# Performance work log

Hardware: AMD Instinct MI355X
Metric: run time of the kernel (lower is better)

The kernel has to match this reference:

```python
import jax, jax.numpy as jnp
import numpy as np

TAU_MEM = 20.0          # tau for both ExpLeak (syn) and LIF (mem)
SPIKE_THRESHOLD = 1.0
WIDTH_GRAD = 0.5        # surrogate gradient width (unused in fwd)
SCALE_GRAD = 1.0


def setup_inputs() -> dict:
    key = jax.random.key(0)
    k1, k2 = jax.random.split(key)
    x = jax.random.normal(k1, (32, 2048, 512, 1), dtype=jnp.float32)
    weight = jax.random.uniform(k2, (1, 1), dtype=jnp.float32)  # Linear(1,1,bias=False) weight (set to scalar `weight` in torch)
    return {"x": x, "weight": weight}


def reference(x, weight):
    # x: (B, T, N, 1); weight: (1, 1)
    alpha = jnp.exp(jnp.asarray(-1.0 / TAU_MEM, dtype=x.dtype))
    i_in = x * weight[0, 0]                      # Linear(1,1,no bias)
    i_in = jnp.moveaxis(i_in, 1, 0)              # (T, B, N, 1) for scan over time

    def step(carry, i_t):
        v_syn, v_mem = carry
        # ExpLeak, norm_input=False: v_syn = alpha*v_syn + input
        v_syn = alpha * v_syn + i_t
        # LIF, norm_input=False: decay then integrate synaptic current
        v_mem = alpha * v_mem + v_syn
        # SingleSpike: at most one spike per step
        spk = (v_mem >= SPIKE_THRESHOLD).astype(v_mem.dtype)
        # MembraneSubtract reset
        v_mem = v_mem - SPIKE_THRESHOLD * spk
        return (v_syn, v_mem), spk

    zeros = jnp.zeros_like(i_in[0])
    _, spikes = jax.lax.scan(step, (zeros, zeros), i_in)
    return jnp.moveaxis(spikes, 0, 1)            # (B, T, N, 1)
```

## Files before the change

kernel.cpp:

```cpp
#include <hip/hip_runtime.h>
#include <math.h>


constexpr int T_ = 2048;
constexpr int N_ = 512;
constexpr int TILE = 64;
constexpr int NTILE = T_ / TILE;
constexpr int NCH = 64;
constexpr int NBUF = 4;

typedef const __attribute__((address_space(1))) void* gas_ptr;
typedef __attribute__((address_space(3))) void* las_ptr;

__global__ __launch_bounds__(128, 1)
void exodus_dma2_kernel(const float* __restrict__ x,
                        const float* __restrict__ wptr,
                        float* __restrict__ out) {
    __shared__ float XBUF[NBUF][TILE][NCH];

    const int blk  = blockIdx.x;
    const int b    = blk >> 3;
    const int n0   = (blk & 7) * NCH;
    const int wave = threadIdx.x >> 6;
    const int lane = threadIdx.x & 63;

    if (wave == 1) {
        const int plane = lane >> 4;
        const int sub   = lane & 15;
        const float* __restrict__ gl =
            x + (size_t)b * T_ * N_ + (size_t)plane * N_ + n0 + sub * 4;

#define ISSUE_TILE(TT)                                                        \
        {                                                                     \
            const float* __restrict__ g_ =                                    \
                gl + (size_t)(TT) * TILE * N_;                                \
            _Pragma("unroll")                                                 \
            for (int j0_ = 0; j0_ < TILE; j0_ += 4) {                         \
                __builtin_amdgcn_global_load_lds(                             \
                    (gas_ptr)(g_ + (size_t)j0_ * N_),                         \
                    (las_ptr)&XBUF[(TT) & (NBUF - 1)][j0_][0], 16, 0, 0);     \
            }                                                                 \
        }

        ISSUE_TILE(0);
        ISSUE_TILE(1);
        __builtin_amdgcn_sched_barrier(0);
        asm volatile("s_waitcnt vmcnt(16)");
        __builtin_amdgcn_sched_barrier(0);
        __builtin_amdgcn_s_barrier();

        for (int t = 0; t < NTILE; ++t) {
            if (t + 2 < NTILE) {
                ISSUE_TILE(t + 2);
                __builtin_amdgcn_sched_barrier(0);
                asm volatile("s_waitcnt vmcnt(16)");
            } else {
                asm volatile("s_waitcnt vmcnt(0)");
            }
            __builtin_amdgcn_sched_barrier(0);
            __builtin_amdgcn_s_barrier();
        }
#undef ISSUE_TILE
    } else {
        const size_t base = (size_t)b * T_ * N_ + (size_t)n0 + lane;
        float* __restrict__ op = out + base;
        const float w = wptr[0];
        const float alpha = (float)exp((double)(-1.0f / 20.0f));
        float vsyn = 0.0f, vmem = 0.0f;

        __builtin_amdgcn_s_barrier();

        for (int t = 0; t < NTILE; ++t) {
            const int bb = t & (NBUF - 1);
            __builtin_amdgcn_sched_barrier(0);

            float xv[TILE];
#pragma unroll
            for (int j = 0; j < TILE; ++j) xv[j] = XBUF[bb][j][lane];

            float* __restrict__ o = op + (size_t)t * TILE * N_;
#pragma unroll
            for (int j = 0; j < TILE; ++j) {
                const float i_t = __fmul_rn(xv[j], w);
                vsyn = __fadd_rn(__fmul_rn(alpha, vsyn), i_t);
                const float va = __fadd_rn(__fmul_rn(alpha, vmem), vsyn);
                const bool fire = (va >= 1.0f);
                __builtin_nontemporal_store(fire ? 1.0f : 0.0f,
                                            o + (size_t)j * N_);
                vmem = fire ? __fsub_rn(va, 1.0f) : va;
            }
            __builtin_amdgcn_sched_barrier(0);
            __builtin_amdgcn_s_barrier();
        }
    }
}

extern "C" void kernel_launch(void* const* d_in, const int* in_sizes, int n_in,
                              void* d_out, int out_size, void* d_ws, size_t ws_size,
                              hipStream_t stream) {
    const float* x = (const float*)d_in[0];
    const float* w = (const float*)d_in[1];
    float* out = (float*)d_out;

    dim3 grid(256);
    dim3 block(128);
    hipLaunchKernelGGL(exodus_dma2_kernel, grid, block, 0, stream, x, w, out);
}
```

Before: 238.2 us.

## Add a dedicated store wave that writes spikes from LDS with float4 stores

Adds a third wave per block. The compute wave now writes spike values into a double-buffered LDS staging area instead of issuing per-element nontemporal global stores. The new wave reads the previous tile from LDS and writes it out as coalesced float4 stores, so stores overlap with compute of the next tile. This costs more LDS, a third wave, and an extra LDS round-trip, and the stores lose the nontemporal hint.

```diff
diff --git a/kernel.cpp b/kernel.cpp
--- a/kernel.cpp
+++ b/kernel.cpp
@@ -12,11 +12,12 @@
 typedef const __attribute__((address_space(1))) void* gas_ptr;
 typedef __attribute__((address_space(3))) void* las_ptr;
 
-__global__ __launch_bounds__(128, 1)
-void exodus_dma2_kernel(const float* __restrict__ x,
-                        const float* __restrict__ wptr,
-                        float* __restrict__ out) {
+__global__ __launch_bounds__(192, 1)
+void exodus_tri_kernel(const float* __restrict__ x,
+                       const float* __restrict__ wptr,
+                       float* __restrict__ out) {
     __shared__ float XBUF[NBUF][TILE][NCH];
+    __shared__ float SBUF[2][TILE][NCH];
 
     const int blk  = blockIdx.x;
     const int b    = blk >> 3;
@@ -61,9 +62,7 @@
             __builtin_amdgcn_s_barrier();
         }
 #undef ISSUE_TILE
-    } else {
-        const size_t base = (size_t)b * T_ * N_ + (size_t)n0 + lane;
-        float* __restrict__ op = out + base;
+    } else if (wave == 0) {
         const float w = wptr[0];
         const float alpha = (float)exp((double)(-1.0f / 20.0f));
         float vsyn = 0.0f, vmem = 0.0f;
@@ -71,26 +70,63 @@
         __builtin_amdgcn_s_barrier();
 
         for (int t = 0; t < NTILE; ++t) {
-            const int bb = t & (NBUF - 1);
+            const int xb = t & (NBUF - 1);
+            const int sb = t & 1;
             __builtin_amdgcn_sched_barrier(0);
 
             float xv[TILE];
 #pragma unroll
-            for (int j = 0; j < TILE; ++j) xv[j] = XBUF[bb][j][lane];
+            for (int j = 0; j < TILE; ++j) xv[j] = XBUF[xb][j][lane];
 
-            float* __restrict__ o = op + (size_t)t * TILE * N_;
 #pragma unroll
             for (int j = 0; j < TILE; ++j) {
                 const float i_t = __fmul_rn(xv[j], w);
                 vsyn = __fadd_rn(__fmul_rn(alpha, vsyn), i_t);
                 const float va = __fadd_rn(__fmul_rn(alpha, vmem), vsyn);
                 const bool fire = (va >= 1.0f);
-                __builtin_nontemporal_store(fire ? 1.0f : 0.0f,
-                                            o + (size_t)j * N_);
+                SBUF[sb][j][lane] = fire ? 1.0f : 0.0f;
                 vmem = fire ? __fsub_rn(va, 1.0f) : va;
             }
             __builtin_amdgcn_sched_barrier(0);
+            asm volatile("s_waitcnt lgkmcnt(0)");
+            __builtin_amdgcn_sched_barrier(0);
             __builtin_amdgcn_s_barrier();
+        }
+    } else {
+        const int plane = lane >> 4;
+        const int sub   = lane & 15;
+        float* __restrict__ ow =
+            out + (size_t)b * T_ * N_ + (size_t)plane * N_ + n0 + sub * 4;
+
+        __builtin_amdgcn_s_barrier();
+
+        for (int t = 0; t < NTILE; ++t) {
+            if (t >= 1) {
+                const int sb = (t - 1) & 1;
+                float4 v[16];
+#pragma unroll
+                for (int k = 0; k < 16; ++k)
+                    v[k] = *(const float4*)&SBUF[sb][4 * k + plane][sub * 4];
+                float* __restrict__ o = ow + (size_t)(t - 1) * TILE * N_;
+#pragma unroll
+                for (int k = 0; k < 16; ++k)
+                    *(float4*)(o + (size_t)(4 * k) * N_) = v[k];
+            }
+            __builtin_amdgcn_sched_barrier(0);
+            asm volatile("s_waitcnt lgkmcnt(0)");
+            __builtin_amdgcn_sched_barrier(0);
+            __builtin_amdgcn_s_barrier();
+        }
+        {
+            const int sb = (NTILE - 1) & 1;
+            float4 v[16];
+#pragma unroll
+            for (int k = 0; k < 16; ++k)
+                v[k] = *(const float4*)&SBUF[sb][4 * k + plane][sub * 4];
+            float* __restrict__ o = ow + (size_t)(NTILE - 1) * TILE * N_;
+#pragma unroll
+            for (int k = 0; k < 16; ++k)
+                *(float4*)(o + (size_t)(4 * k) * N_) = v[k];
         }
     }
 }
@@ -103,6 +139,6 @@
     float* out = (float*)d_out;
 
     dim3 grid(256);
-    dim3 block(128);
-    hipLaunchKernelGGL(exodus_dma2_kernel, grid, block, 0, stream, x, w, out);
+    dim3 block(192);
+    hipLaunchKernelGGL(exodus_tri_kernel, grid, block, 0, stream, x, w, out);
 }
```

New measurement: 245.9 us. 1.03x slower.
